# Optimization experiments

Hardware: AMD Instinct MI355X
Metric: run time of the kernel (lower is better)

Reference implementation:

```python
import jax, jax.numpy as jnp
import numpy as np

MARGIN = 1.0
EPS = 1e-6  # torch F.pairwise_distance default eps, added elementwise to (x - y)
NEG_INF = -1e30
POS_INF = 1e30


def _pairwise_dist_matrix(e):
    # D[i,j] = || e_i - e_j + EPS ||_2, expanded so we never materialize [B,B,D]:
    # ||d + eps||^2 = ||d||^2 + 2*eps*sum(d) + Dfeat*eps^2,  d = e_i - e_j
    sq = jnp.sum(e * e, axis=1)          # [B]
    s = jnp.sum(e, axis=1)               # [B]
    d2 = (sq[:, None] + sq[None, :] - 2.0 * (e @ e.T)
          + 2.0 * EPS * (s[:, None] - s[None, :])
          + e.shape[1] * (EPS * EPS))
    return jnp.sqrt(jnp.maximum(d2, 0.0))  # [B,B]


def _pdist(x, y):
    # F.pairwise_distance(p=2): ||x - y + eps||
    return jnp.sqrt(jnp.sum(jnp.square(x - y + EPS), axis=-1))


def setup_inputs() -> dict:
    B, D = 4096, 128
    key = jax.random.key(0)
    k1, k2, k3, k4 = jax.random.split(key, 4)
    embedding = jax.random.normal(k1, (B, D), dtype=jnp.float32)
    # label space == batch, each label appears exactly once in the batch
    target_idx = jax.random.permutation(k2, B).astype(jnp.int32)
    positive_idxs = jax.random.bernoulli(k3, 0.02, (B, B))  # [B, L] label-space mask
    negative_idxs = jax.random.bernoulli(k4, 0.5, (B, B))
    return {"embedding": embedding, "target_idx": target_idx,
            "positive_idxs": positive_idxs, "negative_idxs": negative_idxs}


def reference(embedding, target_idx, positive_idxs, negative_idxs):
    # Mining happens under no_grad in the original module.
    dm = jax.lax.stop_gradient(_pairwise_dist_matrix(embedding))  # [B,B]
    # batch j is a positive/negative candidate for anchor i iff its label is flagged
    pos_mask = positive_idxs[:, target_idx]  # [B,B] bool
    neg_mask = negative_idxs[:, target_idx]
    pos_idx = jnp.argmax(jnp.where(pos_mask, dm, NEG_INF), axis=1)  # hardest positive
    neg_idx = jnp.argmin(jnp.where(neg_mask, dm, POS_INF), axis=1)  # hardest negative
    valid = jnp.any(pos_mask, axis=1) & jnp.any(neg_mask, axis=1)
    a = embedding
    p = embedding[pos_idx]
    n = embedding[neg_idx]
    ap = _pdist(a, p)
    an = _pdist(a, n)
    pn = _pdist(p, n)
    loss = jax.nn.relu(ap - jnp.minimum(an, pn) + MARGIN)
    w = valid.astype(loss.dtype)
    return jnp.sum(loss * w) / jnp.maximum(jnp.sum(w), 1.0)
```

## Files before the change

### kernel.cpp

```cpp
#include <hip/hip_runtime.h>
#include <stdint.h>

#define BN 4096
#define DD 128
#define EPSF 1e-6f
#define MARGINF 1.0f

typedef unsigned long long ull;
typedef unsigned short ushort;
typedef short short8 __attribute__((ext_vector_type(8)));
typedef float f32x4 __attribute__((ext_vector_type(4)));

__device__ __forceinline__ unsigned int ord_f32(float f) {
    unsigned int u = __float_as_uint(f);
    return (u & 0x80000000u) ? ~u : (u | 0x80000000u);
}
__device__ __forceinline__ ushort bf16_rne(float x) {
    unsigned int u = __float_as_uint(x);
    return (ushort)((u + 0x7FFFu + ((u >> 16) & 1u)) >> 16);
}

__global__ void k_prep(const float* __restrict__ e, const int* __restrict__ tidx,
                       float* __restrict__ sq, float* __restrict__ s,
                       int* __restrict__ inv, ull* __restrict__ pk, ull* __restrict__ nk,
                       unsigned int* __restrict__ ehi, unsigned int* __restrict__ elo) {
    int w = threadIdx.x >> 6, lane = threadIdx.x & 63;
    int row = blockIdx.x * 4 + w;
    float2 v = ((const float2*)(e + (size_t)row * DD))[lane];
    ushort hx = bf16_rne(v.x), hy = bf16_rne(v.y);
    float rx = v.x - __uint_as_float((unsigned int)hx << 16);
    float ry = v.y - __uint_as_float((unsigned int)hy << 16);
    ushort lx = bf16_rne(rx), ly = bf16_rne(ry);
    ehi[row * 64 + lane] = (unsigned int)hx | ((unsigned int)hy << 16);
    elo[row * 64 + lane] = (unsigned int)lx | ((unsigned int)ly << 16);
    float ss = v.x + v.y;
    float qq = v.x * v.x + v.y * v.y;
    #pragma unroll
    for (int off = 32; off > 0; off >>= 1) {
        ss += __shfl_down(ss, off);
        qq += __shfl_down(qq, off);
    }
    if (lane == 0) {
        sq[row] = qq; s[row] = ss;
        inv[tidx[row]] = row;
        pk[row] = 0ULL; nk[row] = 0ULL;
    }
}

__global__ void k_bits(const int* __restrict__ pos, const int* __restrict__ neg,
                       ushort* __restrict__ pb, ushort* __restrict__ nb) {
    const int row = blockIdx.x, t = threadIdx.x;
    const int4* pr = (const int4*)(pos + (size_t)row * BN) + t * 4;
    const int4* nr = (const int4*)(neg + (size_t)row * BN) + t * 4;
    int4 p0 = pr[0], p1 = pr[1], p2 = pr[2], p3 = pr[3];
    int4 n0 = nr[0], n1 = nr[1], n2 = nr[2], n3 = nr[3];
    unsigned int m = 0;
    m |= (p0.x != 0) << 0;  m |= (p0.y != 0) << 1;  m |= (p0.z != 0) << 2;  m |= (p0.w != 0) << 3;
    m |= (p1.x != 0) << 4;  m |= (p1.y != 0) << 5;  m |= (p1.z != 0) << 6;  m |= (p1.w != 0) << 7;
    m |= (p2.x != 0) << 8;  m |= (p2.y != 0) << 9;  m |= (p2.z != 0) << 10; m |= (p2.w != 0) << 11;
    m |= (p3.x != 0) << 12; m |= (p3.y != 0) << 13; m |= (p3.z != 0) << 14; m |= (p3.w != 0) << 15;
    pb[(size_t)row * 256 + t] = (ushort)m;
    m = 0;
    m |= (n0.x != 0) << 0;  m |= (n0.y != 0) << 1;  m |= (n0.z != 0) << 2;  m |= (n0.w != 0) << 3;
    m |= (n1.x != 0) << 4;  m |= (n1.y != 0) << 5;  m |= (n1.z != 0) << 6;  m |= (n1.w != 0) << 7;
    m |= (n2.x != 0) << 8;  m |= (n2.y != 0) << 9;  m |= (n2.z != 0) << 10; m |= (n2.w != 0) << 11;
    m |= (n3.x != 0) << 12; m |= (n3.y != 0) << 13; m |= (n3.z != 0) << 14; m |= (n3.w != 0) << 15;
    nb[(size_t)row * 256 + t] = (ushort)m;
}

__global__ __launch_bounds__(256, 3)
void k_select(const ushort* __restrict__ ehi, const ushort* __restrict__ elo,
              const float* __restrict__ sq, const float* __restrict__ s,
              const int* __restrict__ inv,
              const ull* __restrict__ pbits, const ull* __restrict__ nbits,
              ull* __restrict__ pkey, ull* __restrict__ nkey) {
    __shared__ __align__(16) char smem[36864];
    __shared__ ull pbl[256], nbl[256];
    __shared__ float rjl[128];
    __shared__ int jvs[128];

    ushort* Bh = (ushort*)smem;
    ushort* Bl = (ushort*)(smem + 18432);

    const int tid = threadIdx.x;
    const int lane = tid & 63;
    const int w = tid >> 6, wr = w >> 1, wc = w & 1;
    const int lrow = lane & 15, quad = lane >> 4;
    const int i0 = blockIdx.x * 128, c0 = blockIdx.y * 128;

    if (tid < 128) {
        int j = inv[c0 + tid];
        jvs[tid] = j;
        rjl[tid] = sq[j] - 2.0f * EPSF * s[j];
    }
    {
        int r = tid >> 1, h = tid & 1;
        size_t b = (size_t)(i0 + r) * 64 + (c0 >> 6) + h;
        pbl[tid] = pbits[b];
        nbl[tid] = nbits[b];
    }
    __syncthreads();

    size_t aoff[4];
    #pragma unroll
    for (int rt = 0; rt < 4; rt++)
        aoff[rt] = (size_t)(i0 + wr * 64 + rt * 16 + lrow) * DD + quad * 8;

    f32x4 acc[4][4];
    #pragma unroll
    for (int rt = 0; rt < 4; rt++)
        #pragma unroll
        for (int ct = 0; ct < 4; ct++)
            acc[rt][ct] = (f32x4){0.f, 0.f, 0.f, 0.f};

    for (int kc = 0; kc < 2; kc++) {
        if (kc) __syncthreads();
        #pragma unroll
        for (int it = 0; it < 8; it++) {
            int slot = it * 256 + tid;
            int seg = slot & 7;
            int r = (slot >> 3) & 127;
            int jr = jvs[r];
            const ushort* src = (it < 4) ? ehi : elo;
            int4 v = ((const int4*)(src + (size_t)jr * DD))[kc * 8 + seg];
            ushort* dst = ((it < 4) ? Bh : Bl) + r * 72 + seg * 8;
            *(int4*)dst = v;
        }
        __syncthreads();
        #pragma unroll
        for (int ks = 0; ks < 2; ks++) {
            const int kof = kc * 64 + ks * 32;
            short8 ah[4], al[4];
            #pragma unroll
            for (int rt = 0; rt < 4; rt++) {
                ah[rt] = *(const short8*)(ehi + aoff[rt] + kof);
                al[rt] = *(const short8*)(elo + aoff[rt] + kof);
            }
            #pragma unroll
            for (int ct = 0; ct < 4; ct++) {
                const int bo = (wc * 64 + ct * 16 + lrow) * 72 + ks * 32 + quad * 8;
                short8 bh = *(const short8*)(Bh + bo);
                short8 bl = *(const short8*)(Bl + bo);
                #pragma unroll
                for (int rt = 0; rt < 4; rt++) {
                    acc[rt][ct] = __builtin_amdgcn_mfma_f32_16x16x32_bf16(ah[rt], bh, acc[rt][ct], 0, 0, 0);
                    acc[rt][ct] = __builtin_amdgcn_mfma_f32_16x16x32_bf16(ah[rt], bl, acc[rt][ct], 0, 0, 0);
                    acc[rt][ct] = __builtin_amdgcn_mfma_f32_16x16x32_bf16(al[rt], bh, acc[rt][ct], 0, 0, 0);
                }
            }
        }
    }

    int jcol[4]; float rjc[4];
    #pragma unroll
    for (int ct = 0; ct < 4; ct++) {
        jcol[ct] = jvs[wc * 64 + ct * 16 + lrow];
        rjc[ct] = rjl[wc * 64 + ct * 16 + lrow];
    }
    float bpv[16], bnv[16]; int bpi[16], bni[16];
    #pragma unroll
    for (int k = 0; k < 16; k++) {
        bpv[k] = -3.4e38f; bnv[k] = 3.4e38f;
        bpi[k] = 0x7FFFFFFF; bni[k] = 0x7FFFFFFF;
    }
    #pragma unroll
    for (int rt = 0; rt < 4; rt++)
        #pragma unroll
        for (int t = 0; t < 4; t++) {
            const int slot = rt * 4 + t;
            const int row = wr * 64 + rt * 16 + quad * 4 + t;
            ull pb = pbl[row * 2 + wc] >> lrow;
            ull nb = nbl[row * 2 + wc] >> lrow;
            #pragma unroll
            for (int ct = 0; ct < 4; ct++) {
                float m = rjc[ct] - 2.0f * acc[rt][ct][t];
                int j = jcol[ct];
                if ((pb >> (ct * 16)) & 1ULL) {
                    if (m > bpv[slot] || (m == bpv[slot] && j < bpi[slot])) { bpv[slot] = m; bpi[slot] = j; }
                }
                if ((nb >> (ct * 16)) & 1ULL) {
                    if (m < bnv[slot] || (m == bnv[slot] && j < bni[slot])) { bnv[slot] = m; bni[slot] = j; }
                }
            }
        }

    __syncthreads();
    ull* scrp = (ull*)smem;
    ull* scrn = (ull*)(smem + 16384);
    #pragma unroll
    for (int rt = 0; rt < 4; rt++)
        #pragma unroll
        for (int t = 0; t < 4; t++) {
            const int slot = rt * 4 + t;
            const int row = wr * 64 + rt * 16 + quad * 4 + t;
            ull kp = (bpi[slot] == 0x7FFFFFFF) ? 0ULL
                   : (((ull)ord_f32(bpv[slot]) << 32) | (ull)(0xFFFFFFFFu - (unsigned)bpi[slot]));
            ull kn = (bni[slot] == 0x7FFFFFFF) ? 0ULL
                   : (((ull)(~ord_f32(bnv[slot])) << 32) | (ull)(0xFFFFFFFFu - (unsigned)bni[slot]));
            ull op = __shfl_xor(kp, 8); if (op > kp) kp = op;
            ull on = __shfl_xor(kn, 8); if (on > kn) kn = on;
            if (lrow < 8) {
                scrp[row * 16 + wc * 8 + lrow] = kp;
                scrn[row * 16 + wc * 8 + lrow] = kn;
            }
        }
    __syncthreads();
    if (tid < 128) {
        ull kp = 0ULL, kn = 0ULL;
        for (int k = 0; k < 16; k++) {
            ull v = scrp[tid * 16 + k]; if (v > kp) kp = v;
            v = scrn[tid * 16 + k];     if (v > kn) kn = v;
        }
        if (kp) atomicMax(&pkey[i0 + tid], kp);
        if (kn) atomicMax(&nkey[i0 + tid], kn);
    }
}

__global__ void k_loss(const float* __restrict__ e,
                       const ull* __restrict__ pkey, const ull* __restrict__ nkey,
                       float* __restrict__ partials) {
    int w = threadIdx.x >> 6, lane = threadIdx.x & 63;
    int row = blockIdx.x * 4 + w;
    ull pk = pkey[row], nk = nkey[row];
    float loss = 0.0f, wt = 0.0f;
    if (pk != 0ULL && nk != 0ULL) {
        int pi = (int)(0xFFFFFFFFu - (unsigned)(pk & 0xFFFFFFFFu));
        int ni = (int)(0xFFFFFFFFu - (unsigned)(nk & 0xFFFFFFFFu));
        float2 av = ((const float2*)(e + (size_t)row * DD))[lane];
        float2 pv = ((const float2*)(e + (size_t)pi * DD))[lane];
        float2 nv = ((const float2*)(e + (size_t)ni * DD))[lane];
        float dx, dy;
        dx = av.x - pv.x + EPSF; dy = av.y - pv.y + EPSF;
        float ap2 = dx * dx + dy * dy;
        dx = av.x - nv.x + EPSF; dy = av.y - nv.y + EPSF;
        float an2 = dx * dx + dy * dy;
        dx = pv.x - nv.x + EPSF; dy = pv.y - nv.y + EPSF;
        float pn2 = dx * dx + dy * dy;
        #pragma unroll
        for (int off = 32; off > 0; off >>= 1) {
            ap2 += __shfl_down(ap2, off);
            an2 += __shfl_down(an2, off);
            pn2 += __shfl_down(pn2, off);
        }
        if (lane == 0) {
            float ap = sqrtf(ap2), an = sqrtf(an2), pn = sqrtf(pn2);
            loss = fmaxf(ap - fminf(an, pn) + MARGINF, 0.0f);
            wt = 1.0f;
        }
    }
    __shared__ float sl[4], sw[4];
    if (lane == 0) { sl[w] = loss; sw[w] = wt; }
    __syncthreads();
    if (threadIdx.x == 0) {
        partials[blockIdx.x * 2 + 0] = sl[0] + sl[1] + sl[2] + sl[3];
        partials[blockIdx.x * 2 + 1] = sw[0] + sw[1] + sw[2] + sw[3];
    }
}

__global__ void k_final(const float* __restrict__ partials, float* __restrict__ out) {
    int tid = threadIdx.x;
    float L = 0.0f, W = 0.0f;
    for (int i = 0; i < 4; i++) {
        int idx = tid + i * 256;
        L += partials[idx * 2];
        W += partials[idx * 2 + 1];
    }
    #pragma unroll
    for (int off = 32; off > 0; off >>= 1) {
        L += __shfl_down(L, off);
        W += __shfl_down(W, off);
    }
    __shared__ float sl[4], sw[4];
    int w = tid >> 6, lane = tid & 63;
    if (lane == 0) { sl[w] = L; sw[w] = W; }
    __syncthreads();
    if (tid == 0) {
        float Lt = sl[0] + sl[1] + sl[2] + sl[3];
        float Wt = sw[0] + sw[1] + sw[2] + sw[3];
        out[0] = Lt / fmaxf(Wt, 1.0f);
    }
}

extern "C" void kernel_launch(void* const* d_in, const int* in_sizes, int n_in,
                              void* d_out, int out_size, void* d_ws, size_t ws_size,
                              hipStream_t stream) {
    const float* e    = (const float*)d_in[0];
    const int*   tidx = (const int*)d_in[1];
    const int*   pos  = (const int*)d_in[2];
    const int*   neg  = (const int*)d_in[3];
    float* out = (float*)d_out;

    ull* pkey  = (ull*)d_ws;
    ull* nkey  = pkey + BN;
    ull* pbits = nkey + BN;
    ull* nbits = pbits + BN * 64;
    float* sq  = (float*)(nbits + BN * 64);
    float* s   = sq + BN;
    int* inv   = (int*)(s + BN);
    float* partials = (float*)(inv + BN);
    unsigned int* ehi = (unsigned int*)(partials + 2048);
    unsigned int* elo = ehi + BN * 64;

    k_prep<<<BN / 4, 256, 0, stream>>>(e, tidx, sq, s, inv, pkey, nkey, ehi, elo);
    k_bits<<<BN, 256, 0, stream>>>(pos, neg, (ushort*)pbits, (ushort*)nbits);
    dim3 grid(BN / 128, BN / 128);
    k_select<<<grid, 256, 0, stream>>>((const ushort*)ehi, (const ushort*)elo,
                                       sq, s, inv, pbits, nbits, pkey, nkey);
    k_loss<<<BN / 4, 256, 0, stream>>>(e, pkey, nkey, partials);
    k_final<<<1, 256, 0, stream>>>(partials, out);
}
```

Before: 203.2 us.

## Use single bf16 MFMA product instead of split hi/lo and load full K tile once

Drops the low-order bf16 residual of the embeddings and computes the Gram matrix with one bf16 MFMA per tile instead of three. The whole 128-wide K slab of B is staged into shared memory in one pass, and per-row best-candidate tracking is folded inline to cut register pressure, allowing occupancy hint 4. This removes two thirds of the matrix-core work and half the gather traffic. The cost is reduced distance precision, which can flip near-tie hardest positive/negative selections.

```diff
diff --git a/kernel.cpp b/kernel.cpp
--- a/kernel.cpp
+++ b/kernel.cpp
@@ -23,16 +23,12 @@
 __global__ void k_prep(const float* __restrict__ e, const int* __restrict__ tidx,
                        float* __restrict__ sq, float* __restrict__ s,
                        int* __restrict__ inv, ull* __restrict__ pk, ull* __restrict__ nk,
-                       unsigned int* __restrict__ ehi, unsigned int* __restrict__ elo) {
+                       unsigned int* __restrict__ ehi) {
     int w = threadIdx.x >> 6, lane = threadIdx.x & 63;
     int row = blockIdx.x * 4 + w;
     float2 v = ((const float2*)(e + (size_t)row * DD))[lane];
     ushort hx = bf16_rne(v.x), hy = bf16_rne(v.y);
-    float rx = v.x - __uint_as_float((unsigned int)hx << 16);
-    float ry = v.y - __uint_as_float((unsigned int)hy << 16);
-    ushort lx = bf16_rne(rx), ly = bf16_rne(ry);
     ehi[row * 64 + lane] = (unsigned int)hx | ((unsigned int)hy << 16);
-    elo[row * 64 + lane] = (unsigned int)lx | ((unsigned int)ly << 16);
     float ss = v.x + v.y;
     float qq = v.x * v.x + v.y * v.y;
     #pragma unroll
@@ -68,19 +64,17 @@
     nb[(size_t)row * 256 + t] = (ushort)m;
 }
 
-__global__ __launch_bounds__(256, 3)
-void k_select(const ushort* __restrict__ ehi, const ushort* __restrict__ elo,
+__global__ __launch_bounds__(256, 4)
+void k_select(const ushort* __restrict__ ehi,
               const float* __restrict__ sq, const float* __restrict__ s,
               const int* __restrict__ inv,
               const ull* __restrict__ pbits, const ull* __restrict__ nbits,
               ull* __restrict__ pkey, ull* __restrict__ nkey) {
     __shared__ __align__(16) char smem[36864];
-    __shared__ ull pbl[256], nbl[256];
     __shared__ float rjl[128];
     __shared__ int jvs[128];
 
-    ushort* Bh = (ushort*)smem;
-    ushort* Bl = (ushort*)(smem + 18432);
+    ushort* Bst = (ushort*)smem;
 
     const int tid = threadIdx.x;
     const int lane = tid & 63;
@@ -93,6 +87,51 @@
         jvs[tid] = j;
         rjl[tid] = sq[j] - 2.0f * EPSF * s[j];
     }
+    __syncthreads();
+
+    #pragma unroll
+    for (int it = 0; it < 8; it++) {
+        int slot = it * 256 + tid;
+        int r = slot >> 4, seg16 = slot & 15;
+        int kc = seg16 >> 3, seg = seg16 & 7;
+        int jr = jvs[r];
+        int4 v = ((const int4*)ehi)[(size_t)jr * 16 + seg16];
+        *(int4*)(Bst + (kc * 128 + r) * 72 + seg * 8) = v;
+    }
+    __syncthreads();
+
+    f32x4 acc[4][4];
+    #pragma unroll
+    for (int rt = 0; rt < 4; rt++)
+        #pragma unroll
+        for (int ct = 0; ct < 4; ct++)
+            acc[rt][ct] = (f32x4){0.f, 0.f, 0.f, 0.f};
+
+    size_t abase[4];
+    #pragma unroll
+    for (int rt = 0; rt < 4; rt++)
+        abase[rt] = (size_t)(i0 + wr * 64 + rt * 16 + lrow) * DD + quad * 8;
+
+    #pragma unroll
+    for (int ks = 0; ks < 4; ks++) {
+        const int kc = ks >> 1, ksl = ks & 1;
+        short8 ah[4];
+        #pragma unroll
+        for (int rt = 0; rt < 4; rt++)
+            ah[rt] = *(const short8*)(ehi + abase[rt] + ks * 32);
+        #pragma unroll
+        for (int ct = 0; ct < 4; ct++) {
+            const int bo = (kc * 128 + wc * 64 + ct * 16 + lrow) * 72 + ksl * 32 + quad * 8;
+            short8 bh = *(const short8*)(Bst + bo);
+            #pragma unroll
+            for (int rt = 0; rt < 4; rt++)
+                acc[rt][ct] = __builtin_amdgcn_mfma_f32_16x16x32_bf16(ah[rt], bh, acc[rt][ct], 0, 0, 0);
+        }
+    }
+
+    __syncthreads();
+    ull* pbl = (ull*)smem;
+    ull* nbl = (ull*)(smem + 2048);
     {
         int r = tid >> 1, h = tid & 1;
         size_t b = (size_t)(i0 + r) * 64 + (c0 >> 6) + h;
@@ -101,115 +140,52 @@
     }
     __syncthreads();
 
-    size_t aoff[4];
-    #pragma unroll
-    for (int rt = 0; rt < 4; rt++)
-        aoff[rt] = (size_t)(i0 + wr * 64 + rt * 16 + lrow) * DD + quad * 8;
-
-    f32x4 acc[4][4];
-    #pragma unroll
-    for (int rt = 0; rt < 4; rt++)
-        #pragma unroll
-        for (int ct = 0; ct < 4; ct++)
-            acc[rt][ct] = (f32x4){0.f, 0.f, 0.f, 0.f};
-
-    for (int kc = 0; kc < 2; kc++) {
-        if (kc) __syncthreads();
-        #pragma unroll
-        for (int it = 0; it < 8; it++) {
-            int slot = it * 256 + tid;
-            int seg = slot & 7;
-            int r = (slot >> 3) & 127;
-            int jr = jvs[r];
-            const ushort* src = (it < 4) ? ehi : elo;
-            int4 v = ((const int4*)(src + (size_t)jr * DD))[kc * 8 + seg];
-            ushort* dst = ((it < 4) ? Bh : Bl) + r * 72 + seg * 8;
-            *(int4*)dst = v;
-        }
-        __syncthreads();
-        #pragma unroll
-        for (int ks = 0; ks < 2; ks++) {
-            const int kof = kc * 64 + ks * 32;
-            short8 ah[4], al[4];
-            #pragma unroll
-            for (int rt = 0; rt < 4; rt++) {
-                ah[rt] = *(const short8*)(ehi + aoff[rt] + kof);
-                al[rt] = *(const short8*)(elo + aoff[rt] + kof);
-            }
-            #pragma unroll
-            for (int ct = 0; ct < 4; ct++) {
-                const int bo = (wc * 64 + ct * 16 + lrow) * 72 + ks * 32 + quad * 8;
-                short8 bh = *(const short8*)(Bh + bo);
-                short8 bl = *(const short8*)(Bl + bo);
-                #pragma unroll
-                for (int rt = 0; rt < 4; rt++) {
-                    acc[rt][ct] = __builtin_amdgcn_mfma_f32_16x16x32_bf16(ah[rt], bh, acc[rt][ct], 0, 0, 0);
-                    acc[rt][ct] = __builtin_amdgcn_mfma_f32_16x16x32_bf16(ah[rt], bl, acc[rt][ct], 0, 0, 0);
-                    acc[rt][ct] = __builtin_amdgcn_mfma_f32_16x16x32_bf16(al[rt], bh, acc[rt][ct], 0, 0, 0);
-                }
-            }
-        }
-    }
-
     int jcol[4]; float rjc[4];
     #pragma unroll
     for (int ct = 0; ct < 4; ct++) {
         jcol[ct] = jvs[wc * 64 + ct * 16 + lrow];
         rjc[ct] = rjl[wc * 64 + ct * 16 + lrow];
     }
-    float bpv[16], bnv[16]; int bpi[16], bni[16];
-    #pragma unroll
-    for (int k = 0; k < 16; k++) {
-        bpv[k] = -3.4e38f; bnv[k] = 3.4e38f;
-        bpi[k] = 0x7FFFFFFF; bni[k] = 0x7FFFFFFF;
-    }
+    ull* scrp = (ull*)(smem + 4096);
+    ull* scrn = (ull*)(smem + 20480);
     #pragma unroll
     for (int rt = 0; rt < 4; rt++)
         #pragma unroll
         for (int t = 0; t < 4; t++) {
-            const int slot = rt * 4 + t;
             const int row = wr * 64 + rt * 16 + quad * 4 + t;
             ull pb = pbl[row * 2 + wc] >> lrow;
             ull nb = nbl[row * 2 + wc] >> lrow;
+            float bpv = -3.4e38f, bnv = 3.4e38f;
+            int bpi = 0x7FFFFFFF, bni = 0x7FFFFFFF;
             #pragma unroll
             for (int ct = 0; ct < 4; ct++) {
                 float m = rjc[ct] - 2.0f * acc[rt][ct][t];
                 int j = jcol[ct];
                 if ((pb >> (ct * 16)) & 1ULL) {
-                    if (m > bpv[slot] || (m == bpv[slot] && j < bpi[slot])) { bpv[slot] = m; bpi[slot] = j; }
+                    if (m > bpv || (m == bpv && j < bpi)) { bpv = m; bpi = j; }
                 }
                 if ((nb >> (ct * 16)) & 1ULL) {
-                    if (m < bnv[slot] || (m == bnv[slot] && j < bni[slot])) { bnv[slot] = m; bni[slot] = j; }
+                    if (m < bnv || (m == bnv && j < bni)) { bnv = m; bni = j; }
                 }
             }
-        }
-
-    __syncthreads();
-    ull* scrp = (ull*)smem;
-    ull* scrn = (ull*)(smem + 16384);
-    #pragma unroll
-    for (int rt = 0; rt < 4; rt++)
-        #pragma unroll
-        for (int t = 0; t < 4; t++) {
-            const int slot = rt * 4 + t;
-            const int row = wr * 64 + rt * 16 + quad * 4 + t;
-            ull kp = (bpi[slot] == 0x7FFFFFFF) ? 0ULL
-                   : (((ull)ord_f32(bpv[slot]) << 32) | (ull)(0xFFFFFFFFu - (unsigned)bpi[slot]));
-            ull kn = (bni[slot] == 0x7FFFFFFF) ? 0ULL
-                   : (((ull)(~ord_f32(bnv[slot])) << 32) | (ull)(0xFFFFFFFFu - (unsigned)bni[slot]));
+            ull kp = (bpi == 0x7FFFFFFF) ? 0ULL
+                   : (((ull)ord_f32(bpv) << 32) | (ull)(0xFFFFFFFFu - (unsigned)bpi));
+            ull kn = (bni == 0x7FFFFFFF) ? 0ULL
+                   : (((ull)(~ord_f32(bnv)) << 32) | (ull)(0xFFFFFFFFu - (unsigned)bni));
             ull op = __shfl_xor(kp, 8); if (op > kp) kp = op;
             ull on = __shfl_xor(kn, 8); if (on > kn) kn = on;
             if (lrow < 8) {
-                scrp[row * 16 + wc * 8 + lrow] = kp;
-                scrn[row * 16 + wc * 8 + lrow] = kn;
+                scrp[(wc * 8 + lrow) * 128 + row] = kp;
+                scrn[(wc * 8 + lrow) * 128 + row] = kn;
             }
         }
     __syncthreads();
     if (tid < 128) {
         ull kp = 0ULL, kn = 0ULL;
+        #pragma unroll
         for (int k = 0; k < 16; k++) {
-            ull v = scrp[tid * 16 + k]; if (v > kp) kp = v;
-            v = scrn[tid * 16 + k];     if (v > kn) kn = v;
+            ull v = scrp[k * 128 + tid]; if (v > kp) kp = v;
+            v = scrn[k * 128 + tid];     if (v > kn) kn = v;
         }
         if (kp) atomicMax(&pkey[i0 + tid], kp);
         if (kn) atomicMax(&nkey[i0 + tid], kn);
@@ -299,13 +275,12 @@
     int* inv   = (int*)(s + BN);
     float* partials = (float*)(inv + BN);
     unsigned int* ehi = (unsigned int*)(partials + 2048);
-    unsigned int* elo = ehi + BN * 64;
-
-    k_prep<<<BN / 4, 256, 0, stream>>>(e, tidx, sq, s, inv, pkey, nkey, ehi, elo);
+
+    k_prep<<<BN / 4, 256, 0, stream>>>(e, tidx, sq, s, inv, pkey, nkey, ehi);
     k_bits<<<BN, 256, 0, stream>>>(pos, neg, (ushort*)pbits, (ushort*)nbits);
     dim3 grid(BN / 128, BN / 128);
-    k_select<<<grid, 256, 0, stream>>>((const ushort*)ehi, (const ushort*)elo,
-                                       sq, s, inv, pbits, nbits, pkey, nkey);
+    k_select<<<grid, 256, 0, stream>>>((const ushort*)ehi, sq, s, inv,
+                                       pbits, nbits, pkey, nkey);
     k_loss<<<BN / 4, 256, 0, stream>>>(e, pkey, nkey, partials);
     k_final<<<1, 256, 0, stream>>>(partials, out);
 }
```

Result: faster. 185.7 us (-8.6%).
